# Optimization experiments

Measured on AMD Instinct MI355X. Metric: run time of the kernel, lower is better.

## Reference

```python
import jax, jax.numpy as jnp
import numpy as np

K = 4
TEMPERATURE = 30.0


def setup_inputs() -> dict:
    key = jax.random.key(0)
    ks = jax.random.split(key, 6)
    B, C, H, W_sp = 32, 128, 56, 56
    Cout, kh, kw = 128, 3, 3
    Cred = max(C // 4, 1)
    x = jax.random.normal(ks[0], (B, C, H, W_sp), dtype=jnp.float32)
    # K parallel conv kernels + biases (fan-in scaled init)
    fan = C * kh * kw
    W = jax.random.normal(ks[1], (K, Cout, C, kh, kw), dtype=jnp.float32) / np.sqrt(fan)
    b = jax.random.normal(ks[2], (K, Cout), dtype=jnp.float32) * 0.01
    # attention branch: 1x1 convs == dense on pooled features
    aw1 = jax.random.normal(ks[3], (Cred, C), dtype=jnp.float32) / np.sqrt(C)
    aw2 = jax.random.normal(ks[4], (K, Cred), dtype=jnp.float32) / np.sqrt(Cred)
    return {"x": x, "W": W, "b": b, "aw1": aw1, "aw2": aw2}


def reference(x, W, b, aw1, aw2):
    # attention: global avg pool -> 1x1 conv (dense) -> relu -> 1x1 conv -> softmax(logits/T)
    pooled = jnp.mean(x, axis=(2, 3))                       # [B, C]
    h1 = jax.nn.relu(jnp.einsum('bc,rc->br', pooled, aw1))  # [B, Cred]
    logits = jnp.einsum('br,kr->bk', h1, aw2)               # [B, K]
    attn = jax.nn.softmax(logits / TEMPERATURE, axis=1)     # [B, K]

    pad = 1
    out = None
    for i in range(K):  # fixed small K, structurally distinct kernels
        yi = jax.lax.conv_general_dilated(
            x, W[i], window_strides=(1, 1), padding=[(pad, pad), (pad, pad)],
            dimension_numbers=('NCHW', 'OIHW', 'NCHW'))
        yi = yi + b[i][None, :, None, None]
        yi = yi * attn[:, i][:, None, None, None]
        out = yi if out is None else out + yi
    return out
```

## Files before the change

### kernel.cpp

```cpp
#include <hip/hip_runtime.h>
#include <hip/hip_bf16.h>
#include <stdint.h>

typedef __bf16 bf16x8 __attribute__((ext_vector_type(8)));
typedef float  f32x4  __attribute__((ext_vector_type(4)));
typedef unsigned short u16x8 __attribute__((ext_vector_type(8)));
typedef unsigned int   u32x4 __attribute__((ext_vector_type(4)));

#define NB 32
#define NC 128
#define NH 56
#define NW 56
#define NK 4
#define NCO 128
#define NCR 32
#define NHW 3136
#define TEMPER 30.0f

#define WS_ATTN   0u
#define WS_BC     4096u
#define WS_ROWSUM 65536u
#define WS_WC     1048576u
#define WS_XT     10485760u

__global__ void xt_kernel(const float* __restrict__ x, __hip_bfloat16* __restrict__ xt,
                          float* __restrict__ rowsum) {
  __shared__ float lds[58 * 133];
  int xcd = blockIdx.x & 7;
  int j   = blockIdx.x >> 3;
  int b   = xcd * 4 + j / 58;
  int hp  = j % 58;
  int blk = b * 58 + hp;
  int h = hp - 1;
  bool hin = (h >= 0) && (h < NH);
  int tid = threadIdx.x;
  if (hin) {
    const float* xrow = x + ((size_t)b * NC) * NHW + (size_t)h * NW;
    for (int i = tid; i < 128 * 14; i += 256) {
      int c = i / 14;
      int w4 = (i - c * 14) * 4;
      float4 v = *(const float4*)(xrow + (size_t)c * NHW + w4);
      int base = (w4 + 1) * 133 + c;
      lds[base]         = v.x;
      lds[base + 133]   = v.y;
      lds[base + 2*133] = v.z;
      lds[base + 3*133] = v.w;
    }
  }
  __syncthreads();
  __hip_bfloat16* orow = xt + (size_t)blk * (58 * 128);
  for (int i = tid; i < 58 * 16; i += 256) {
    int wp = i >> 4;
    int cg = (i & 15) << 3;
    u16x8 o;
    if (!hin || wp == 0 || wp == 57) {
      o = (u16x8)0;
    } else {
      const float* src = lds + wp * 133 + cg;
      #pragma unroll
      for (int jx = 0; jx < 8; ++jx) {
        union { __hip_bfloat16 b; unsigned short u; } cv;
        cv.b = __float2bfloat16(src[jx]);
        o[jx] = cv.u;
      }
    }
    *(u16x8*)(orow + wp * 128 + cg) = o;
  }
  if (hin && tid < 128) {
    float s = 0.f;
    #pragma unroll 8
    for (int wp = 1; wp <= 56; ++wp) s += lds[wp * 133 + tid];
    rowsum[(size_t)blk * 128 + tid] = s;
  }
}

__global__ void attn_kernel(const float* __restrict__ rowsum, const float* __restrict__ aw1,
                            const float* __restrict__ aw2, const float* __restrict__ bias,
                            float* __restrict__ attn, float* __restrict__ bc_out) {
  int b = blockIdx.x;
  __shared__ float sp[NC], h1[NCR], at[NK];
  int t = threadIdx.x;
  if (t < NC) {
    float s = 0.f;
    for (int hp = 1; hp <= 56; ++hp) s += rowsum[((size_t)b * 58 + hp) * 128 + t];
    sp[t] = s * (1.0f / (float)NHW);
  }
  __syncthreads();
  if (t < NCR) {
    float s = 0.f;
    for (int c = 0; c < NC; ++c) s += aw1[t*NC + c] * sp[c];
    h1[t] = s > 0.f ? s : 0.f;
  }
  __syncthreads();
  if (t == 0) {
    float lg[NK], mx = -1e30f;
    for (int k = 0; k < NK; ++k) {
      float s = 0.f;
      for (int r = 0; r < NCR; ++r) s += aw2[k*NCR + r] * h1[r];
      lg[k] = s * (1.0f/TEMPER);
      mx = fmaxf(mx, lg[k]);
    }
    float den = 0.f, e[NK];
    for (int k = 0; k < NK; ++k) { e[k] = expf(lg[k]-mx); den += e[k]; }
    float inv = 1.0f/den;
    for (int k = 0; k < NK; ++k) { at[k] = e[k]*inv; attn[b*NK+k] = at[k]; }
  }
  __syncthreads();
  if (t < NCO) {
    float s = 0.f;
    for (int k = 0; k < NK; ++k) s += at[k] * bias[k*NCO + t];
    bc_out[b*NCO + t] = s;
  }
}

__global__ void combine_kernel(const float* __restrict__ W, const float* __restrict__ attn,
                               __hip_bfloat16* __restrict__ wc) {
  int gid = blockIdx.x;
  int bg  = gid >> 6;
  int tcell = (gid & 63) * 256 + threadIdx.x;
  int co = tcell >> 7, ci = tcell & 127;
  float w[4][9];
  const float* wp = W + ((size_t)co * 128 + ci) * 9;
  #pragma unroll
  for (int k = 0; k < 4; ++k)
    #pragma unroll
    for (int j = 0; j < 9; ++j)
      w[k][j] = wp[(size_t)k * 147456 + j];
  for (int b = bg * 8; b < bg * 8 + 8; ++b) {
    float a0 = attn[b*4+0], a1 = attn[b*4+1], a2 = attn[b*4+2], a3 = attn[b*4+3];
    #pragma unroll
    for (int j = 0; j < 9; ++j) {
      float v = a0*w[0][j] + a1*w[1][j] + a2*w[2][j] + a3*w[3][j];
      wc[(((size_t)b*9 + j) * 128 + co) * 128 + ci] = __float2bfloat16(v);
    }
  }
}

#define RS 2368
#define CS 40
#define AKS 5120

#define GLOAD16(src, dst) \
  __builtin_amdgcn_global_load_lds( \
    (const __attribute__((address_space(1))) unsigned int*)(src), \
    (__attribute__((address_space(3))) unsigned int*)(dst), 16, 0, 0)

__global__ __launch_bounds__(512, 2) void conv_kernel(
    const unsigned short* __restrict__ xt,
    const unsigned short* __restrict__ wc,
    const float* __restrict__ bc,
    float* __restrict__ out) {
  __shared__ __align__(16) unsigned short lds_a[9*AKS];
  __shared__ __align__(16) unsigned short lds_b[10*RS];
  const int tid  = threadIdx.x;
  const int lane = tid & 63;
  const int wv   = tid >> 6;
  const int wm   = wv >> 2;
  const int wn   = wv & 3;
  const int bid  = blockIdx.x;
  const int xcd  = bid & 7;
  const int jj   = bid >> 3;
  const int b    = xcd*4 + jj/7;
  const int r0   = (jj % 7) * 8;
  const int li   = lane & 15;
  const int kg   = lane >> 4;

  int srcB[6];
  #pragma unroll
  for (int i = 0; i < 6; ++i) {
    int q = i*512 + tid;
    int r = q / 296;
    int sl = q - r*296;
    int col = sl / 5;
    int part = sl - col*5;
    srcB[i] = (q < 2960 && col < 58 && part < 4)
              ? ((r0 + r)*58 + col)*128 + part*8 : -1;
  }
  int aS[9], aD[9];
  #pragma unroll
  for (int i = 0; i < 9; ++i) {
    int s = i*512 + tid;
    int khw = s >> 9;
    int co  = (s & 511) >> 2;
    int part = s & 3;
    aS[i] = (khw*128 + co)*128 + part*8;
    aD[i] = (khw*128 + co)*40 + part*8;
  }

  int xoff[7];
  #pragma unroll
  for (int f = 0; f < 7; ++f) {
    int pos = wn*112 + f*16 + li;
    int rB = pos / 56;
    int cB = pos - rB*56;
    xoff[f] = rB*RS + cB*CS + kg*8;
  }
  const int aRead = (wm*64 + li)*40 + kg*8;

  const f32x4 vzero = {0.f, 0.f, 0.f, 0.f};
  f32x4 acc[4][7];
  #pragma unroll
  for (int mo = 0; mo < 4; ++mo)
    #pragma unroll
    for (int f = 0; f < 7; ++f) acc[mo][f] = vzero;

  const unsigned short* xtg = xt + (size_t)b*(58*58*128);
  const unsigned short* wcg = wc + (size_t)b*(9*128*128);

  for (int cc = 0; cc < 4; ++cc) {
    u32x4 areg[9];
    #pragma unroll
    for (int i = 0; i < 9; ++i)
      areg[i] = *(const u32x4*)(wcg + aS[i] + cc*32);

    __syncthreads();

    #pragma unroll
    for (int i = 0; i < 6; ++i)
      if (srcB[i] >= 0)
        GLOAD16(xtg + srcB[i] + cc*32, lds_b + (i*512 + wv*64)*8);
    #pragma unroll
    for (int i = 0; i < 9; ++i)
      *(u32x4*)(lds_a + aD[i]) = areg[i];

    __syncthreads();

    #pragma unroll
    for (int khw = 0; khw < 9; ++khw) {
      const int kh = khw / 3;
      const int kw = khw - kh*3;
      bf16x8 af[4];
      #pragma unroll
      for (int mo = 0; mo < 4; ++mo)
        af[mo] = *(const bf16x8*)(lds_a + khw*AKS + aRead + mo*640);
      const int koff = kh*RS + kw*CS;
      bf16x8 bfr[7];
      #pragma unroll
      for (int f = 0; f < 7; ++f)
        bfr[f] = *(const bf16x8*)(lds_b + xoff[f] + koff);
      __builtin_amdgcn_s_setprio(1);
      #pragma unroll
      for (int mo = 0; mo < 4; ++mo)
        #pragma unroll
        for (int f = 0; f < 7; ++f)
          acc[mo][f] = __builtin_amdgcn_mfma_f32_16x16x32_bf16(af[mo], bfr[f], acc[mo][f], 0, 0, 0);
      __builtin_amdgcn_s_setprio(0);
    }
  }

  float* ob = out + (size_t)b*NCO*NHW;
  #pragma unroll
  for (int mo = 0; mo < 4; ++mo) {
    #pragma unroll
    for (int rg = 0; rg < 4; ++rg) {
      const int co = wm*64 + mo*16 + kg*4 + rg;
      const float bv = bc[b*NCO + co];
      float* orow = ob + (size_t)co*NHW;
      #pragma unroll
      for (int f = 0; f < 7; ++f) {
        int pos = wn*112 + f*16 + li;
        int rB = pos / 56;
        int cB = pos - rB*56;
        orow[(r0 + rB)*56 + cB] = acc[mo][f][rg] + bv;
      }
    }
  }
}

extern "C" void kernel_launch(void* const* d_in, const int* in_sizes, int n_in,
                              void* d_out, int out_size, void* d_ws, size_t ws_size,
                              hipStream_t stream) {
  const float* x   = (const float*)d_in[0];
  const float* W   = (const float*)d_in[1];
  const float* bia = (const float*)d_in[2];
  const float* aw1 = (const float*)d_in[3];
  const float* aw2 = (const float*)d_in[4];
  float* out = (float*)d_out;
  char* ws = (char*)d_ws;
  float* attn   = (float*)(ws + WS_ATTN);
  float* bcm    = (float*)(ws + WS_BC);
  float* rowsum = (float*)(ws + WS_ROWSUM);
  __hip_bfloat16* wc = (__hip_bfloat16*)(ws + WS_WC);
  __hip_bfloat16* xt = (__hip_bfloat16*)(ws + WS_XT);

  xt_kernel<<<NB*58, 256, 0, stream>>>(x, xt, rowsum);
  attn_kernel<<<NB, 128, 0, stream>>>(rowsum, aw1, aw2, bia, attn, bcm);
  combine_kernel<<<256, 256, 0, stream>>>(W, attn, wc);
  conv_kernel<<<224, 512, 0, stream>>>((const unsigned short*)xt,
                                       (const unsigned short*)wc, bcm, out);
}
```

Baseline: 66.41 us.

## Double-buffer conv LDS staging via async global-to-LDS loads and coalesce weight combine

The conv kernel now double-buffers both the activation tile and the weight tile in LDS. Weights are split into per-kh slices and loaded with global_load_lds directly, so the next slice's copy overlaps the current MFMA work instead of going through registers between two barriers. The combine kernel stages W in shared memory and writes 8 contiguous bf16 per thread, replacing scattered 2-byte stores. This adds more barriers (one per kh step) and changes the weight LDS row pitch from 40 to 32, which may raise bank conflicts. The larger LDS footprint may also reduce occupancy.

```diff
diff --git a/kernel.cpp b/kernel.cpp
--- a/kernel.cpp
+++ b/kernel.cpp
@@ -5,7 +5,6 @@
 typedef __bf16 bf16x8 __attribute__((ext_vector_type(8)));
 typedef float  f32x4  __attribute__((ext_vector_type(4)));
 typedef unsigned short u16x8 __attribute__((ext_vector_type(8)));
-typedef unsigned int   u32x4 __attribute__((ext_vector_type(4)));
 
 #define NB 32
 #define NC 128
@@ -115,30 +114,40 @@
 
 __global__ void combine_kernel(const float* __restrict__ W, const float* __restrict__ attn,
                                __hip_bfloat16* __restrict__ wc) {
-  int gid = blockIdx.x;
-  int bg  = gid >> 6;
-  int tcell = (gid & 63) * 256 + threadIdx.x;
-  int co = tcell >> 7, ci = tcell & 127;
-  float w[4][9];
-  const float* wp = W + ((size_t)co * 128 + ci) * 9;
+  __shared__ float wlds[4*576];
+  __shared__ float alds[128];
+  int g = blockIdx.x, tid = threadIdx.x;
+  int co = g >> 1, cig0 = (g & 1) * 64;
+  const float* wbase = W + (size_t)co*1152 + cig0*9;
   #pragma unroll
   for (int k = 0; k < 4; ++k)
+    for (int i = tid; i < 576; i += 256)
+      wlds[k*576 + i] = wbase[(size_t)k*147456 + i];
+  if (tid < 128) alds[tid] = attn[tid];
+  __syncthreads();
+  int b  = tid >> 3;
+  int c8 = (tid & 7) * 8;
+  float a0 = alds[b*4+0], a1 = alds[b*4+1], a2 = alds[b*4+2], a3 = alds[b*4+3];
+  #pragma unroll
+  for (int j = 0; j < 9; ++j) {
+    u16x8 o;
     #pragma unroll
-    for (int j = 0; j < 9; ++j)
-      w[k][j] = wp[(size_t)k * 147456 + j];
-  for (int b = bg * 8; b < bg * 8 + 8; ++b) {
-    float a0 = attn[b*4+0], a1 = attn[b*4+1], a2 = attn[b*4+2], a3 = attn[b*4+3];
-    #pragma unroll
-    for (int j = 0; j < 9; ++j) {
-      float v = a0*w[0][j] + a1*w[1][j] + a2*w[2][j] + a3*w[3][j];
-      wc[(((size_t)b*9 + j) * 128 + co) * 128 + ci] = __float2bfloat16(v);
-    }
+    for (int q = 0; q < 8; ++q) {
+      int idx = (c8 + q)*9 + j;
+      float v = a0*wlds[idx] + a1*wlds[576+idx] + a2*wlds[1152+idx] + a3*wlds[1728+idx];
+      union { __hip_bfloat16 b; unsigned short u; } cv;
+      cv.b = __float2bfloat16(v);
+      o[q] = cv.u;
+    }
+    *(u16x8*)((unsigned short*)wc + (((size_t)b*9 + j)*128 + co)*128 + cig0 + c8) = o;
   }
 }
 
 #define RS 2368
 #define CS 40
-#define AKS 5120
+#define BROWS 10
+#define BBUF (BROWS*RS)
+#define ABUF (3*128*32)
 
 #define GLOAD16(src, dst) \
   __builtin_amdgcn_global_load_lds( \
@@ -150,8 +159,8 @@
     const unsigned short* __restrict__ wc,
     const float* __restrict__ bc,
     float* __restrict__ out) {
-  __shared__ __align__(16) unsigned short lds_a[9*AKS];
-  __shared__ __align__(16) unsigned short lds_b[10*RS];
+  __shared__ __align__(16) unsigned short lds_b[2*BBUF];
+  __shared__ __align__(16) unsigned short lds_a[2*ABUF];
   const int tid  = threadIdx.x;
   const int lane = tid & 63;
   const int wv   = tid >> 6;
@@ -176,15 +185,14 @@
     srcB[i] = (q < 2960 && col < 58 && part < 4)
               ? ((r0 + r)*58 + col)*128 + part*8 : -1;
   }
-  int aS[9], aD[9];
-  #pragma unroll
-  for (int i = 0; i < 9; ++i) {
-    int s = i*512 + tid;
-    int khw = s >> 9;
-    int co  = (s & 511) >> 2;
-    int part = s & 3;
-    aS[i] = (khw*128 + co)*128 + part*8;
-    aD[i] = (khw*128 + co)*40 + part*8;
+  int srcA[3];
+  #pragma unroll
+  for (int i = 0; i < 3; ++i) {
+    int c = i*512 + tid;
+    int khwL = c >> 9;
+    int co   = (c & 511) >> 2;
+    int part = c & 3;
+    srcA[i] = (khwL*128 + co)*128 + part*8;
   }
 
   int xoff[7];
@@ -195,7 +203,7 @@
     int cB = pos - rB*56;
     xoff[f] = rB*RS + cB*CS + kg*8;
   }
-  const int aRead = (wm*64 + li)*40 + kg*8;
+  const int aRead = (wm*64 + li)*32 + kg*8;
 
   const f32x4 vzero = {0.f, 0.f, 0.f, 0.f};
   f32x4 acc[4][7];
@@ -207,45 +215,58 @@
   const unsigned short* xtg = xt + (size_t)b*(58*58*128);
   const unsigned short* wcg = wc + (size_t)b*(9*128*128);
 
+  #define STAGE_B(bufidx, cc) do { \
+    unsigned short* dbase = lds_b + (bufidx)*BBUF + wv*512; \
+    _Pragma("unroll") \
+    for (int i = 0; i < 6; ++i) { \
+      if (srcB[i] >= 0) \
+        GLOAD16(xtg + srcB[i] + (cc)*32, dbase + i*4096); \
+    } \
+  } while (0)
+
+  #define STAGE_A(bufidx, cc, kh) do { \
+    unsigned short* dbase = lds_a + (bufidx)*ABUF + wv*512; \
+    _Pragma("unroll") \
+    for (int i = 0; i < 3; ++i) \
+      GLOAD16(wcg + (kh)*49152 + srcA[i] + (cc)*32, dbase + i*4096); \
+  } while (0)
+
+  STAGE_B(0, 0);
+  STAGE_A(0, 0, 0);
+  __syncthreads();
+
+  int cura = 0, curb = 0;
   for (int cc = 0; cc < 4; ++cc) {
-    u32x4 areg[9];
-    #pragma unroll
-    for (int i = 0; i < 9; ++i)
-      areg[i] = *(const u32x4*)(wcg + aS[i] + cc*32);
-
-    __syncthreads();
-
-    #pragma unroll
-    for (int i = 0; i < 6; ++i)
-      if (srcB[i] >= 0)
-        GLOAD16(xtg + srcB[i] + cc*32, lds_b + (i*512 + wv*64)*8);
-    #pragma unroll
-    for (int i = 0; i < 9; ++i)
-      *(u32x4*)(lds_a + aD[i]) = areg[i];
-
-    __syncthreads();
-
-    #pragma unroll
-    for (int khw = 0; khw < 9; ++khw) {
-      const int kh = khw / 3;
-      const int kw = khw - kh*3;
-      bf16x8 af[4];
+    for (int kh = 0; kh < 3; ++kh) {
+      if (kh < 2)      STAGE_A(cura ^ 1, cc, kh + 1);
+      else if (cc < 3) STAGE_A(cura ^ 1, cc + 1, 0);
+      if (kh == 0 && cc < 3) STAGE_B(curb ^ 1, cc + 1);
+
+      const unsigned short* pa = lds_a + cura*ABUF;
+      const unsigned short* pb = lds_b + curb*BBUF;
       #pragma unroll
-      for (int mo = 0; mo < 4; ++mo)
-        af[mo] = *(const bf16x8*)(lds_a + khw*AKS + aRead + mo*640);
-      const int koff = kh*RS + kw*CS;
-      bf16x8 bfr[7];
-      #pragma unroll
-      for (int f = 0; f < 7; ++f)
-        bfr[f] = *(const bf16x8*)(lds_b + xoff[f] + koff);
-      __builtin_amdgcn_s_setprio(1);
-      #pragma unroll
-      for (int mo = 0; mo < 4; ++mo)
+      for (int kwl = 0; kwl < 3; ++kwl) {
+        bf16x8 af[4];
+        #pragma unroll
+        for (int mo = 0; mo < 4; ++mo)
+          af[mo] = *(const bf16x8*)(pa + kwl*4096 + aRead + mo*512);
+        const int koff = kh*RS + kwl*CS;
+        bf16x8 bfr[7];
         #pragma unroll
         for (int f = 0; f < 7; ++f)
-          acc[mo][f] = __builtin_amdgcn_mfma_f32_16x16x32_bf16(af[mo], bfr[f], acc[mo][f], 0, 0, 0);
-      __builtin_amdgcn_s_setprio(0);
-    }
+          bfr[f] = *(const bf16x8*)(pb + xoff[f] + koff);
+        __builtin_amdgcn_s_setprio(1);
+        #pragma unroll
+        for (int mo = 0; mo < 4; ++mo)
+          #pragma unroll
+          for (int f = 0; f < 7; ++f)
+            acc[mo][f] = __builtin_amdgcn_mfma_f32_16x16x32_bf16(af[mo], bfr[f], acc[mo][f], 0, 0, 0);
+        __builtin_amdgcn_s_setprio(0);
+      }
+      __syncthreads();
+      cura ^= 1;
+    }
+    curb ^= 1;
   }
 
   float* ob = out + (size_t)b*NCO*NHW;
```

Result: slower. 77.20 us (+16.3%).

## Load conv weights directly to LDS and double-buffer fragment reads across taps

Applied to the files above, without the earlier changes.

The weight tile now goes straight from global memory into LDS through global_load_lds instead of being staged in registers, so the LDS row stride for A drops from 40 to 32 (unpadded). The per-tap loop is software pipelined with two fragment register sets, so the LDS reads for the next tap overlap the MFMAs of the current one. The leading barrier is skipped on the first chunk and the setprio hints are removed. Risks are LDS bank conflicts on the unpadded A layout and higher register pressure from the two fragment sets under the 512x2 launch bounds.

```diff
diff --git a/kernel.cpp b/kernel.cpp
--- a/kernel.cpp
+++ b/kernel.cpp
@@ -5,7 +5,6 @@
 typedef __bf16 bf16x8 __attribute__((ext_vector_type(8)));
 typedef float  f32x4  __attribute__((ext_vector_type(4)));
 typedef unsigned short u16x8 __attribute__((ext_vector_type(8)));
-typedef unsigned int   u32x4 __attribute__((ext_vector_type(4)));
 
 #define NB 32
 #define NC 128
@@ -138,7 +137,8 @@
 
 #define RS 2368
 #define CS 40
-#define AKS 5120
+#define BBUF (10*RS)
+#define ABUF (9*128*32)
 
 #define GLOAD16(src, dst) \
   __builtin_amdgcn_global_load_lds( \
@@ -150,8 +150,8 @@
     const unsigned short* __restrict__ wc,
     const float* __restrict__ bc,
     float* __restrict__ out) {
-  __shared__ __align__(16) unsigned short lds_a[9*AKS];
-  __shared__ __align__(16) unsigned short lds_b[10*RS];
+  __shared__ __align__(16) unsigned short lds_a[ABUF];
+  __shared__ __align__(16) unsigned short lds_b[BBUF];
   const int tid  = threadIdx.x;
   const int lane = tid & 63;
   const int wv   = tid >> 6;
@@ -176,15 +176,14 @@
     srcB[i] = (q < 2960 && col < 58 && part < 4)
               ? ((r0 + r)*58 + col)*128 + part*8 : -1;
   }
-  int aS[9], aD[9];
+  int srcA[9];
   #pragma unroll
   for (int i = 0; i < 9; ++i) {
-    int s = i*512 + tid;
-    int khw = s >> 9;
-    int co  = (s & 511) >> 2;
-    int part = s & 3;
-    aS[i] = (khw*128 + co)*128 + part*8;
-    aD[i] = (khw*128 + co)*40 + part*8;
+    int c = i*512 + tid;
+    int khw  = c >> 9;
+    int co   = (c & 511) >> 2;
+    int part = c & 3;
+    srcA[i] = (khw*128 + co)*128 + part*8;
   }
 
   int xoff[7];
@@ -195,7 +194,7 @@
     int cB = pos - rB*56;
     xoff[f] = rB*RS + cB*CS + kg*8;
   }
-  const int aRead = (wm*64 + li)*40 + kg*8;
+  const int aRead = (wm*64 + li)*32 + kg*8;
 
   const f32x4 vzero = {0.f, 0.f, 0.f, 0.f};
   f32x4 acc[4][7];
@@ -207,45 +206,55 @@
   const unsigned short* xtg = xt + (size_t)b*(58*58*128);
   const unsigned short* wcg = wc + (size_t)b*(9*128*128);
 
+  #define LOADFRAG(AF, BF, khw) do { \
+    const int kh_ = (khw)/3, kw_ = (khw)-kh_*3; \
+    _Pragma("unroll") \
+    for (int mo = 0; mo < 4; ++mo) \
+      AF[mo] = *(const bf16x8*)(lds_a + (khw)*4096 + aRead + mo*512); \
+    const int koff_ = kh_*RS + kw_*CS; \
+    _Pragma("unroll") \
+    for (int f = 0; f < 7; ++f) \
+      BF[f] = *(const bf16x8*)(lds_b + xoff[f] + koff_); \
+  } while (0)
+
+  #define DOMFMA(AF, BF) do { \
+    _Pragma("unroll") \
+    for (int mo = 0; mo < 4; ++mo) \
+      _Pragma("unroll") \
+      for (int f = 0; f < 7; ++f) \
+        acc[mo][f] = __builtin_amdgcn_mfma_f32_16x16x32_bf16(AF[mo], BF[f], acc[mo][f], 0, 0, 0); \
+  } while (0)
+
   for (int cc = 0; cc < 4; ++cc) {
-    u32x4 areg[9];
+    if (cc > 0) __syncthreads();
     #pragma unroll
     for (int i = 0; i < 9; ++i)
-      areg[i] = *(const u32x4*)(wcg + aS[i] + cc*32);
-
-    __syncthreads();
-
+      GLOAD16(wcg + srcA[i] + cc*32, lds_a + (i*512 + wv*64)*8);
     #pragma unroll
     for (int i = 0; i < 6; ++i)
       if (srcB[i] >= 0)
         GLOAD16(xtg + srcB[i] + cc*32, lds_b + (i*512 + wv*64)*8);
-    #pragma unroll
-    for (int i = 0; i < 9; ++i)
-      *(u32x4*)(lds_a + aD[i]) = areg[i];
-
     __syncthreads();
 
-    #pragma unroll
-    for (int khw = 0; khw < 9; ++khw) {
-      const int kh = khw / 3;
-      const int kw = khw - kh*3;
-      bf16x8 af[4];
-      #pragma unroll
-      for (int mo = 0; mo < 4; ++mo)
-        af[mo] = *(const bf16x8*)(lds_a + khw*AKS + aRead + mo*640);
-      const int koff = kh*RS + kw*CS;
-      bf16x8 bfr[7];
-      #pragma unroll
-      for (int f = 0; f < 7; ++f)
-        bfr[f] = *(const bf16x8*)(lds_b + xoff[f] + koff);
-      __builtin_amdgcn_s_setprio(1);
-      #pragma unroll
-      for (int mo = 0; mo < 4; ++mo)
-        #pragma unroll
-        for (int f = 0; f < 7; ++f)
-          acc[mo][f] = __builtin_amdgcn_mfma_f32_16x16x32_bf16(af[mo], bfr[f], acc[mo][f], 0, 0, 0);
-      __builtin_amdgcn_s_setprio(0);
-    }
+    bf16x8 afE[4], bfE[7], afO[4], bfO[7];
+    LOADFRAG(afE, bfE, 0);
+    LOADFRAG(afO, bfO, 1);
+    DOMFMA(afE, bfE);
+    LOADFRAG(afE, bfE, 2);
+    DOMFMA(afO, bfO);
+    LOADFRAG(afO, bfO, 3);
+    DOMFMA(afE, bfE);
+    LOADFRAG(afE, bfE, 4);
+    DOMFMA(afO, bfO);
+    LOADFRAG(afO, bfO, 5);
+    DOMFMA(afE, bfE);
+    LOADFRAG(afE, bfE, 6);
+    DOMFMA(afO, bfO);
+    LOADFRAG(afO, bfO, 7);
+    DOMFMA(afE, bfE);
+    LOADFRAG(afE, bfE, 8);
+    DOMFMA(afO, bfO);
+    DOMFMA(afE, bfE);
   }
 
   float* ob = out + (size_t)b*NCO*NHW;
```

After: 66.85 us. No clear change (+0.7%).
